# Optimization experiments

Measured on AMD Instinct MI355X. Metric: run time of the kernel, lower is better.

Reference implementation:

```python
import jax, jax.numpy as jnp
import numpy as np

B, S, E, H = 64, 1024, 256, 1024  # batch, seq_len, d_embed_word (=proj_size), d_hidden


def setup_inputs() -> dict:
    key = jax.random.key(0)
    ks = jax.random.split(key, 11)
    s = 1.0 / np.sqrt(H)  # PyTorch LSTM init: U(-1/sqrt(H), 1/sqrt(H))
    u = lambda k, shape: jax.random.uniform(k, shape, jnp.float32, -s, s)
    return {
        "x": jax.random.normal(ks[0], (B, S, E), jnp.float32),
        # forward direction
        "W_ih_f": u(ks[1], (4 * H, E)),
        "W_hh_f": u(ks[2], (4 * H, E)),  # hidden input is the projected state (dim E)
        "b_ih_f": u(ks[3], (4 * H,)),
        "b_hh_f": u(ks[4], (4 * H,)),
        "W_hr_f": u(ks[5], (E, H)),  # projection weight (proj_size, hidden_size)
        # backward direction
        "W_ih_b": u(ks[6], (4 * H, E)),
        "W_hh_b": u(ks[7], (4 * H, E)),
        "b_ih_b": u(ks[8], (4 * H,)),
        "b_hh_b": u(ks[9], (4 * H,)),
        "W_hr_b": u(ks[10], (E, H)),
    }


def _lstm_dir(x, W_ih, W_hh, b_ih, b_hh, W_hr, reverse):
    """Single-direction LSTM with projection (PyTorch proj_size semantics).
    x: (B, S, E) -> returns (B, S, proj) with proj = W_hr.shape[0]."""
    Bsz = x.shape[0]
    Hd = W_hr.shape[1]
    P = W_hr.shape[0]
    # big input GEMM once, outside the recurrence: (B, S, 4H)
    xg = jnp.einsum('bse,ge->bsg', x, W_ih) + b_ih + b_hh
    xg = jnp.swapaxes(xg, 0, 1)  # (S, B, 4H)
    if reverse:
        xg = xg[::-1]

    def step(carry, gx):
        h, c = carry  # h: (B, P) projected state, c: (B, H)
        g = gx + h @ W_hh.T  # (B, 4H)
        i, f, gg, o = jnp.split(g, 4, axis=-1)  # PyTorch gate order i,f,g,o
        i = jax.nn.sigmoid(i)
        f = jax.nn.sigmoid(f)
        gg = jnp.tanh(gg)
        o = jax.nn.sigmoid(o)
        c = f * c + i * gg
        h = (o * jnp.tanh(c)) @ W_hr.T  # projection to (B, P)
        return (h, c), h

    h0 = jnp.zeros((Bsz, P), x.dtype)
    c0 = jnp.zeros((Bsz, Hd), x.dtype)
    _, hs = jax.lax.scan(step, (h0, c0), xg)  # hs: (S, B, P)
    if reverse:
        hs = hs[::-1]
    return jnp.swapaxes(hs, 0, 1)  # (B, S, P)


def reference(x, W_ih_f, W_hh_f, b_ih_f, b_hh_f, W_hr_f,
              W_ih_b, W_hh_b, b_ih_b, b_hh_b, W_hr_b):
    # Single bidirectional LSTM layer with proj_size (the only runnable
    # configuration of WordLSTM; see notes). Output: (B, S, 2*E).
    fwd = _lstm_dir(x, W_ih_f, W_hh_f, b_ih_f, b_hh_f, W_hr_f, reverse=False)
    bwd = _lstm_dir(x, W_ih_b, W_hh_b, b_ih_b, b_hh_b, W_hr_b, reverse=True)
    return jnp.concatenate([fwd, bwd], axis=-1)
```

## Files before the change

kernel.cpp:

```cpp
#include <hip/hip_runtime.h>


#define NS 1024
#define NE 256
#define NH 1024
#define NP 256
#define MB 16
#define NTH 256
#define TEAMS 8
#define TWGS 32

typedef __attribute__((ext_vector_type(8))) short bf16x8;
typedef __attribute__((ext_vector_type(4))) float f32x4;
typedef __attribute__((ext_vector_type(2))) float f32x2;

#define WS_FLAGS  0
#define WS_ABORT  65536
#define WS_HHI    65792
#define WS_HLO    (WS_HHI + 65536)
#define WS_ACTHI  (WS_HLO + 65536)
#define WS_ACTLO  (WS_ACTHI + 262144)
#define WS_END    (WS_ACTLO + 262144)
#define WS_ZERO   WS_ACTHI

#define WAITV0 asm volatile("s_waitcnt vmcnt(0)" ::: "memory")
#define SBAR0  __builtin_amdgcn_sched_barrier(0)

__device__ __forceinline__ unsigned short f2bf_rne(float f){
  unsigned u = __builtin_bit_cast(unsigned, f);
  u += 0x7fffu + ((u >> 16) & 1u);
  return (unsigned short)(u >> 16);
}
__device__ __forceinline__ unsigned short f2bf_tr(float f){
  return (unsigned short)(__builtin_bit_cast(unsigned, f) >> 16);
}
__device__ __forceinline__ float bf2f(unsigned short h){
  unsigned u = ((unsigned)h) << 16;
  return __builtin_bit_cast(float, u);
}
__device__ __forceinline__ f32x4 MFMA(bf16x8 a, bf16x8 b, f32x4 c){
  return __builtin_amdgcn_mfma_f32_16x16x32_bf16(a, b, c, 0, 0, 0);
}
__device__ __forceinline__ float sigmf(float x){ return 1.0f / (1.0f + __expf(-x)); }
__device__ __forceinline__ float tanhfast(float x){
  x = fminf(fmaxf(x, -15.0f), 15.0f);
  float t = __expf(2.0f * x);
  return (t - 1.0f) / (t + 1.0f);
}

__device__ __forceinline__ void st32_llc(unsigned* p, unsigned v){
  asm volatile("global_store_dword %0, %1, off sc0 sc1" :: "v"(p), "v"(v) : "memory");
}
__device__ __forceinline__ void st16_llc(unsigned short* p, unsigned v){
  asm volatile("global_store_short %0, %1, off sc0 sc1" :: "v"(p), "v"(v) : "memory");
}
__device__ __forceinline__ unsigned ld32_llc(const unsigned* p){
  unsigned v;
  asm volatile("global_load_dword %0, %1, off sc0 sc1\n\ts_waitcnt vmcnt(0)"
               : "=v"(v) : "v"(p) : "memory");
  return v;
}
__device__ __forceinline__ bf16x8 ldx4_llc(const unsigned short* p){
  bf16x8 v;
  asm volatile("global_load_dwordx4 %0, %1, off sc0 sc1" : "=v"(v) : "v"(p));
  return v;
}

__device__ __forceinline__ void wait_flags(const unsigned* flags, unsigned tgt,
                                           unsigned* abortf){
  if (tgt == 0u) return;
  const unsigned* myp = flags + (threadIdx.x & 31) * 32;
  unsigned it = 0;
  for(;;){
    unsigned v = ld32_llc(myp);
    if (__ballot(v >= tgt) == ~0ULL) break;
    if ((++it & 63u) == 0u){
      if (ld32_llc(abortf) != 0u) return;
      if (it > 200000u){
        st32_llc(abortf, 1u);
        return;
      }
    }
  }
}

struct Params {
  const float* x;
  const float* Wih_f; const float* Whh_f; const float* bih_f; const float* bhh_f; const float* Whr_f;
  const float* Wih_b; const float* Whh_b; const float* bih_b; const float* bhh_b; const float* Whr_b;
  float* out;
  unsigned char* ws;
};

__launch_bounds__(NTH, 1)
__global__ void lstm_kernel(Params p){
  __shared__ float Gred[4*4*16*18];
  __shared__ float G2red[4*16*18];

  const int tid  = threadIdx.x;
  const int w    = tid >> 6;
  const int lane = tid & 63;
  const int rl   = lane & 15;
  const int kgrp = lane >> 4;

  const int bid = blockIdx.x;
  const int tm  = bid & 7;
  const int wg  = bid >> 3;
  const int dir = tm >> 2;
  const int bg  = tm & 3;

  const float* Wih = dir ? p.Wih_b : p.Wih_f;
  const float* Whh = dir ? p.Whh_b : p.Whh_f;
  const float* bih = dir ? p.bih_b : p.bih_f;
  const float* bhh = dir ? p.bhh_b : p.bhh_f;
  const float* Whr = dir ? p.Whr_b : p.Whr_f;

  unsigned* act_flags = (unsigned*)(p.ws + WS_FLAGS + tm*8192);
  unsigned* h_flags   = (unsigned*)(p.ws + WS_FLAGS + tm*8192 + 4096);
  unsigned* my_act_flag = act_flags + wg*32;
  unsigned* my_h_flag   = h_flags   + wg*32;
  unsigned* abortf  = (unsigned*)(p.ws + WS_ABORT);
  unsigned short* h_hi   = (unsigned short*)(p.ws + WS_HHI)   + tm*MB*NP;
  unsigned short* h_lo   = (unsigned short*)(p.ws + WS_HLO)   + tm*MB*NP;
  unsigned short* act_hi = (unsigned short*)(p.ws + WS_ACTHI) + tm*MB*NH;
  unsigned short* act_lo = (unsigned short*)(p.ws + WS_ACTLO) + tm*MB*NH;

  const int hb = w & 1;
  const int kh = w >> 1;

  const float* Wsel = kh ? Wih : Whh;
  bf16x8 whi[4][8], wlo[4][8];
  #pragma unroll
  for (int g = 0; g < 4; ++g){
    const float* Wrow = Wsel + (size_t)(g*NH + wg*32 + hb*16 + rl)*NE;
    #pragma unroll
    for (int kt = 0; kt < 8; ++kt){
      const int k0 = kt*32 + kgrp*8;
      #pragma unroll
      for (int j = 0; j < 8; ++j){
        float v = Wrow[k0 + j];
        unsigned short hv = f2bf_rne(v);
        whi[g][kt][j] = (short)hv;
        wlo[g][kt][j] = (short)f2bf_rne(v - bf2f(hv));
      }
    }
  }

  bf16x8 whrh[8], whrl[8];
  #pragma unroll
  for (int q = 0; q < 8; ++q){
    const int k0 = w*256 + q*32 + kgrp*8;
    #pragma unroll
    for (int j = 0; j < 8; ++j){
      float v = (rl < 8) ? Whr[(size_t)(wg*8 + rl)*NH + k0 + j] : 0.0f;
      unsigned short hv = f2bf_rne(v);
      whrh[q][j] = (short)hv;
      whrl[q][j] = (short)f2bf_rne(v - bf2f(hv));
    }
  }

  float bias[4];
  #pragma unroll
  for (int g = 0; g < 4; ++g){
    const int grow = g*NH + wg*32 + hb*16 + rl;
    bias[g] = (kh == 0) ? (bih[grow] + bhh[grow]) : 0.0f;
  }

  const int bh2   = w >> 1;
  const int idx0  = lane * 2;
  const int gb16  = bh2*8 + (idx0 >> 4);
  const int ghidx = idx0 & 15;
  float c0 = 0.0f, c1 = 0.0f;

  for (int s = 0; s < NS; ++s){
    const int sx = dir ? (NS-1-s) : s;

    f32x4 acc[4];
    #pragma unroll
    for (int g = 0; g < 4; ++g) acc[g] = (f32x4){bias[g], bias[g], bias[g], bias[g]};

    if (kh == 0){
      wait_flags(h_flags, (unsigned)s, abortf);
      #pragma unroll
      for (int gk = 0; gk < 2; ++gk){
        bf16x8 ah[4], al[4];
        #pragma unroll
        for (int kt2 = 0; kt2 < 4; ++kt2){
          const int k0 = (gk*4 + kt2)*32 + kgrp*8;
          ah[kt2] = ldx4_llc(h_hi + rl*NP + k0);
          al[kt2] = ldx4_llc(h_lo + rl*NP + k0);
        }
        WAITV0; SBAR0;
        #pragma unroll
        for (int kt2 = 0; kt2 < 4; ++kt2){
          const int kt = gk*4 + kt2;
          #pragma unroll
          for (int g = 0; g < 4; ++g){
            acc[g] = MFMA(ah[kt2], whi[g][kt], acc[g]);
            acc[g] = MFMA(al[kt2], whi[g][kt], acc[g]);
            acc[g] = MFMA(ah[kt2], wlo[g][kt], acc[g]);
          }
        }
      }
    } else {
      const float* xb = p.x + ((size_t)(bg*16 + rl)*NS + (size_t)sx)*NE;
      #pragma unroll
      for (int kt = 0; kt < 8; ++kt){
        const int k0 = kt*32 + kgrp*8;
        f32x4 va = *(const f32x4*)(xb + k0);
        f32x4 vb = *(const f32x4*)(xb + k0 + 4);
        bf16x8 ahi, alo;
        #pragma unroll
        for (int j = 0; j < 4; ++j){
          unsigned short h1 = f2bf_tr(va[j]);
          ahi[j]   = (short)h1; alo[j]   = (short)f2bf_tr(va[j] - bf2f(h1));
          unsigned short h2 = f2bf_tr(vb[j]);
          ahi[j+4] = (short)h2; alo[j+4] = (short)f2bf_tr(vb[j] - bf2f(h2));
        }
        #pragma unroll
        for (int g = 0; g < 4; ++g){
          acc[g] = MFMA(ahi, whi[g][kt], acc[g]);
          acc[g] = MFMA(alo, whi[g][kt], acc[g]);
          acc[g] = MFMA(ahi, wlo[g][kt], acc[g]);
        }
      }
    }

    #pragma unroll
    for (int g = 0; g < 4; ++g){
      #pragma unroll
      for (int r = 0; r < 4; ++r)
        Gred[(((kh*2+hb)*4 + g)*16 + (kgrp*4 + r))*18 + rl] = acc[g][r];
    }
    __syncthreads();

    {
      unsigned short ahi16[2], alo16[2];
      float gs[4][2];
      #pragma unroll
      for (int g = 0; g < 4; ++g){
        f32x2 a0 = *(const f32x2*)&Gred[((hb*4 + g)*16 + gb16)*18 + ghidx];
        f32x2 a1 = *(const f32x2*)&Gred[(((2+hb)*4 + g)*16 + gb16)*18 + ghidx];
        gs[g][0] = a0[0] + a1[0];
        gs[g][1] = a0[1] + a1[1];
      }
      #pragma unroll
      for (int j = 0; j < 2; ++j){
        float iv = sigmf(gs[0][j]);
        float fv = sigmf(gs[1][j]);
        float gv = tanhfast(gs[2][j]);
        float ov = sigmf(gs[3][j]);
        float c  = fv * (j ? c1 : c0) + iv * gv;
        if (j) c1 = c; else c0 = c;
        float a  = ov * tanhfast(c);
        ahi16[j] = f2bf_tr(a);
        alo16[j] = f2bf_tr(a - bf2f(ahi16[j]));
      }
      const unsigned colg = (unsigned)(wg*32 + hb*16 + ghidx);
      st32_llc((unsigned*)(act_hi + gb16*NH + colg),
               (unsigned)ahi16[0] | ((unsigned)ahi16[1] << 16));
      st32_llc((unsigned*)(act_lo + gb16*NH + colg),
               (unsigned)alo16[0] | ((unsigned)alo16[1] << 16));
    }
    WAITV0;
    __syncthreads();
    if (tid == 0)
      st32_llc(my_act_flag, (unsigned)(s+1));
    wait_flags(act_flags, (unsigned)(s+1), abortf);

    f32x4 acc2 = (f32x4){0.0f, 0.0f, 0.0f, 0.0f};
    #pragma unroll
    for (int gq = 0; gq < 2; ++gq){
      bf16x8 ah[4], al[4];
      #pragma unroll
      for (int q2 = 0; q2 < 4; ++q2){
        const int k0 = w*256 + (gq*4 + q2)*32 + kgrp*8;
        ah[q2] = ldx4_llc(act_hi + rl*NH + k0);
        al[q2] = ldx4_llc(act_lo + rl*NH + k0);
      }
      WAITV0; SBAR0;
      #pragma unroll
      for (int q2 = 0; q2 < 4; ++q2){
        const int q = gq*4 + q2;
        acc2 = MFMA(ah[q2], whrh[q], acc2);
        acc2 = MFMA(al[q2], whrh[q], acc2);
        acc2 = MFMA(ah[q2], whrl[q], acc2);
      }
    }
    #pragma unroll
    for (int r = 0; r < 4; ++r)
      G2red[(w*16 + (kgrp*4 + r))*18 + rl] = acc2[r];
    __syncthreads();

    float vout[4];
    if (w == 0){
      #pragma unroll
      for (int r = 0; r < 4; ++r){
        const int b16 = kgrp*4 + r;
        float v = G2red[(0*16 + b16)*18 + rl] + G2red[(1*16 + b16)*18 + rl]
                + G2red[(2*16 + b16)*18 + rl] + G2red[(3*16 + b16)*18 + rl];
        vout[r] = v;
        if (rl < 8){
          const int pcol = wg*8 + rl;
          unsigned short hh = f2bf_tr(v);
          st16_llc(h_hi + b16*NP + pcol, (unsigned)hh);
          st16_llc(h_lo + b16*NP + pcol, (unsigned)f2bf_tr(v - bf2f(hh)));
        }
      }
      WAITV0;
      if (lane == 0)
        st32_llc(my_h_flag, (unsigned)(s+1));

      if (rl < 8){
        const int pcol = wg*8 + rl;
        #pragma unroll
        for (int r = 0; r < 4; ++r){
          const int bglob = bg*16 + kgrp*4 + r;
          p.out[((size_t)bglob*NS + (size_t)sx)*512 + dir*256 + pcol] = vout[r];
        }
      }
    }
  }
}

extern "C" void kernel_launch(void* const* d_in, const int* in_sizes, int n_in,
                              void* d_out, int out_size, void* d_ws, size_t ws_size,
                              hipStream_t stream) {
  (void)in_sizes; (void)n_in; (void)out_size; (void)ws_size;

  Params prm;
  prm.x     = (const float*)d_in[0];
  prm.Wih_f = (const float*)d_in[1];
  prm.Whh_f = (const float*)d_in[2];
  prm.bih_f = (const float*)d_in[3];
  prm.bhh_f = (const float*)d_in[4];
  prm.Whr_f = (const float*)d_in[5];
  prm.Wih_b = (const float*)d_in[6];
  prm.Whh_b = (const float*)d_in[7];
  prm.bih_b = (const float*)d_in[8];
  prm.bhh_b = (const float*)d_in[9];
  prm.Whr_b = (const float*)d_in[10];
  prm.out   = (float*)d_out;
  prm.ws    = (unsigned char*)d_ws;

  hipMemsetAsync(d_ws, 0, WS_ZERO, stream);

  lstm_kernel<<<dim3(TEAMS*TWGS), dim3(NTH), 0, stream>>>(prm);
}
```

Baseline: 10.90 ms.

## Tile inter-WG exchange buffers and narrow act-flag waits per wave

Changes the global scratch layout for the h and activation exchange buffers so that each workgroup's slice is contiguous and each 16-byte lane load maps to one 8-column by 16-batch tile. Each wave of the projection stage now waits only on the 8 producer flags for its own K-range instead of all 32 workgroups, which shortens the barrier critical path. All eight loads are issued before a single wait rather than in two batches of four. The cost is more live VGPRs and a layout that every producer and consumer must index the same way.

```diff
diff --git a/kernel.cpp b/kernel.cpp
--- a/kernel.cpp
+++ b/kernel.cpp
@@ -48,26 +48,26 @@
   return (t - 1.0f) / (t + 1.0f);
 }
 
-__device__ __forceinline__ void st32_llc(unsigned* p, unsigned v){
+__device__ __forceinline__ void st32_llc(void* p, unsigned v){
   asm volatile("global_store_dword %0, %1, off sc0 sc1" :: "v"(p), "v"(v) : "memory");
 }
-__device__ __forceinline__ void st16_llc(unsigned short* p, unsigned v){
+__device__ __forceinline__ void st16_llc(void* p, unsigned v){
   asm volatile("global_store_short %0, %1, off sc0 sc1" :: "v"(p), "v"(v) : "memory");
 }
-__device__ __forceinline__ unsigned ld32_llc(const unsigned* p){
+__device__ __forceinline__ unsigned ld32_llc(const void* p){
   unsigned v;
   asm volatile("global_load_dword %0, %1, off sc0 sc1\n\ts_waitcnt vmcnt(0)"
                : "=v"(v) : "v"(p) : "memory");
   return v;
 }
-__device__ __forceinline__ bf16x8 ldx4_llc(const unsigned short* p){
+__device__ __forceinline__ bf16x8 ldx4_llc(const void* p){
   bf16x8 v;
   asm volatile("global_load_dwordx4 %0, %1, off sc0 sc1" : "=v"(v) : "v"(p));
   return v;
 }
 
-__device__ __forceinline__ void wait_flags(const unsigned* flags, unsigned tgt,
-                                           unsigned* abortf){
+__device__ __forceinline__ void wait_flags32(const unsigned* flags, unsigned tgt,
+                                             unsigned* abortf){
   if (tgt == 0u) return;
   const unsigned* myp = flags + (threadIdx.x & 31) * 32;
   unsigned it = 0;
@@ -76,10 +76,21 @@
     if (__ballot(v >= tgt) == ~0ULL) break;
     if ((++it & 63u) == 0u){
       if (ld32_llc(abortf) != 0u) return;
-      if (it > 200000u){
-        st32_llc(abortf, 1u);
-        return;
-      }
+      if (it > 200000u){ st32_llc(abortf, 1u); return; }
+    }
+  }
+}
+__device__ __forceinline__ void wait_flags8(const unsigned* base8, unsigned tgt,
+                                            unsigned* abortf){
+  if (tgt == 0u) return;
+  const unsigned* myp = base8 + (threadIdx.x & 7) * 32;
+  unsigned it = 0;
+  for(;;){
+    unsigned v = ld32_llc(myp);
+    if (__ballot(v >= tgt) == ~0ULL) break;
+    if ((++it & 63u) == 0u){
+      if (ld32_llc(abortf) != 0u) return;
+      if (it > 200000u){ st32_llc(abortf, 1u); return; }
     }
   }
 }
@@ -120,10 +131,10 @@
   unsigned* my_act_flag = act_flags + wg*32;
   unsigned* my_h_flag   = h_flags   + wg*32;
   unsigned* abortf  = (unsigned*)(p.ws + WS_ABORT);
-  unsigned short* h_hi   = (unsigned short*)(p.ws + WS_HHI)   + tm*MB*NP;
-  unsigned short* h_lo   = (unsigned short*)(p.ws + WS_HLO)   + tm*MB*NP;
-  unsigned short* act_hi = (unsigned short*)(p.ws + WS_ACTHI) + tm*MB*NH;
-  unsigned short* act_lo = (unsigned short*)(p.ws + WS_ACTLO) + tm*MB*NH;
+  unsigned char* h_hi   = p.ws + WS_HHI   + tm*8192;
+  unsigned char* h_lo   = p.ws + WS_HLO   + tm*8192;
+  unsigned char* act_hi = p.ws + WS_ACTHI + tm*32768;
+  unsigned char* act_lo = p.ws + WS_ACTLO + tm*32768;
 
   const int hb = w & 1;
   const int kh = w >> 1;
@@ -172,6 +183,8 @@
   const int ghidx = idx0 & 15;
   float c0 = 0.0f, c1 = 0.0f;
 
+  const int fo = kgrp*256 + rl*16;
+
   for (int s = 0; s < NS; ++s){
     const int sx = dir ? (NS-1-s) : s;
 
@@ -180,26 +193,21 @@
     for (int g = 0; g < 4; ++g) acc[g] = (f32x4){bias[g], bias[g], bias[g], bias[g]};
 
     if (kh == 0){
-      wait_flags(h_flags, (unsigned)s, abortf);
-      #pragma unroll
-      for (int gk = 0; gk < 2; ++gk){
-        bf16x8 ah[4], al[4];
+      wait_flags32(h_flags, (unsigned)s, abortf);
+      bf16x8 ah[8], al[8];
+      #pragma unroll
+      for (int kt = 0; kt < 8; ++kt){
+        ah[kt] = ldx4_llc(h_hi + kt*1024 + fo);
+        al[kt] = ldx4_llc(h_lo + kt*1024 + fo);
+      }
+      WAITV0; SBAR0;
+      #pragma unroll
+      for (int kt = 0; kt < 8; ++kt){
         #pragma unroll
-        for (int kt2 = 0; kt2 < 4; ++kt2){
-          const int k0 = (gk*4 + kt2)*32 + kgrp*8;
-          ah[kt2] = ldx4_llc(h_hi + rl*NP + k0);
-          al[kt2] = ldx4_llc(h_lo + rl*NP + k0);
-        }
-        WAITV0; SBAR0;
-        #pragma unroll
-        for (int kt2 = 0; kt2 < 4; ++kt2){
-          const int kt = gk*4 + kt2;
-          #pragma unroll
-          for (int g = 0; g < 4; ++g){
-            acc[g] = MFMA(ah[kt2], whi[g][kt], acc[g]);
-            acc[g] = MFMA(al[kt2], whi[g][kt], acc[g]);
-            acc[g] = MFMA(ah[kt2], wlo[g][kt], acc[g]);
-          }
+        for (int g = 0; g < 4; ++g){
+          acc[g] = MFMA(ah[kt], whi[g][kt], acc[g]);
+          acc[g] = MFMA(al[kt], whi[g][kt], acc[g]);
+          acc[g] = MFMA(ah[kt], wlo[g][kt], acc[g]);
         }
       }
     } else {
@@ -256,35 +264,31 @@
         ahi16[j] = f2bf_tr(a);
         alo16[j] = f2bf_tr(a - bf2f(ahi16[j]));
       }
-      const unsigned colg = (unsigned)(wg*32 + hb*16 + ghidx);
-      st32_llc((unsigned*)(act_hi + gb16*NH + colg),
-               (unsigned)ahi16[0] | ((unsigned)ahi16[1] << 16));
-      st32_llc((unsigned*)(act_lo + gb16*NH + colg),
-               (unsigned)alo16[0] | ((unsigned)alo16[1] << 16));
+      const unsigned colg  = (unsigned)(wg*32 + hb*16 + ghidx);
+      const unsigned abyte = (colg >> 3)*256 + (unsigned)gb16*16 + (colg & 7)*2;
+      st32_llc(act_hi + abyte, (unsigned)ahi16[0] | ((unsigned)ahi16[1] << 16));
+      st32_llc(act_lo + abyte, (unsigned)alo16[0] | ((unsigned)alo16[1] << 16));
     }
     WAITV0;
     __syncthreads();
     if (tid == 0)
       st32_llc(my_act_flag, (unsigned)(s+1));
-    wait_flags(act_flags, (unsigned)(s+1), abortf);
+    wait_flags8(act_flags + w*256, (unsigned)(s+1), abortf);
 
     f32x4 acc2 = (f32x4){0.0f, 0.0f, 0.0f, 0.0f};
-    #pragma unroll
-    for (int gq = 0; gq < 2; ++gq){
-      bf16x8 ah[4], al[4];
-      #pragma unroll
-      for (int q2 = 0; q2 < 4; ++q2){
-        const int k0 = w*256 + (gq*4 + q2)*32 + kgrp*8;
-        ah[q2] = ldx4_llc(act_hi + rl*NH + k0);
-        al[q2] = ldx4_llc(act_lo + rl*NH + k0);
+    {
+      bf16x8 bh[8], bl[8];
+      #pragma unroll
+      for (int q = 0; q < 8; ++q){
+        bh[q] = ldx4_llc(act_hi + w*8192 + q*1024 + fo);
+        bl[q] = ldx4_llc(act_lo + w*8192 + q*1024 + fo);
       }
       WAITV0; SBAR0;
       #pragma unroll
-      for (int q2 = 0; q2 < 4; ++q2){
-        const int q = gq*4 + q2;
-        acc2 = MFMA(ah[q2], whrh[q], acc2);
-        acc2 = MFMA(al[q2], whrh[q], acc2);
-        acc2 = MFMA(ah[q2], whrl[q], acc2);
+      for (int q = 0; q < 8; ++q){
+        acc2 = MFMA(bh[q], whrh[q], acc2);
+        acc2 = MFMA(bl[q], whrh[q], acc2);
+        acc2 = MFMA(bh[q], whrl[q], acc2);
       }
     }
     #pragma unroll
@@ -301,10 +305,9 @@
                 + G2red[(2*16 + b16)*18 + rl] + G2red[(3*16 + b16)*18 + rl];
         vout[r] = v;
         if (rl < 8){
-          const int pcol = wg*8 + rl;
           unsigned short hh = f2bf_tr(v);
-          st16_llc(h_hi + b16*NP + pcol, (unsigned)hh);
-          st16_llc(h_lo + b16*NP + pcol, (unsigned)f2bf_tr(v - bf2f(hh)));
+          st16_llc(h_hi + wg*256 + b16*16 + rl*2, (unsigned)hh);
+          st16_llc(h_lo + wg*256 + b16*16 + rl*2, (unsigned)f2bf_tr(v - bf2f(hh)));
         }
       }
       WAITV0;
```

New measurement: 9.108 ms. 16.5% less time.
